# Kernel optimization log

Measured on AMD Instinct MI355X. Metric: run time of the kernel, lower is better.

## Reference

```python
import jax, jax.numpy as jnp
import numpy as np

N_NODES = 1395
NEG_SLOPE = 0.2


def gcn_conv(x, edge_index, W, b):
    # PyG GCNConv: add self-loops, symmetric deg^{-1/2} normalization,
    # out[i] = sum_j norm_ij * (x W)[j] + b
    N = x.shape[0]
    loop = jnp.arange(N, dtype=edge_index.dtype)
    src = jnp.concatenate([edge_index[0], loop])
    dst = jnp.concatenate([edge_index[1], loop])
    xw = x @ W  # [N, out]
    deg = jax.ops.segment_sum(jnp.ones_like(dst, dtype=x.dtype), dst, num_segments=N)
    dinv = jnp.where(deg > 0, deg ** -0.5, 0.0)
    norm = dinv[src] * dinv[dst]  # [E+N]
    out = jax.ops.segment_sum(xw[src] * norm[:, None], dst, num_segments=N)
    return out + b


def leaky_relu(x):
    return jnp.where(x >= 0, x, NEG_SLOPE * x)


def linear(v, W, b):
    # torch Linear on 1D vector: W @ v + b, W is [out, in]
    return W @ v + b


def conv2d(x, w, b):
    # x: [N,C,H,W], w: [O,I,kh,kw], valid padding, stride 1
    y = jax.lax.conv_general_dilated(
        x, w, window_strides=(1, 1), padding='VALID',
        dimension_numbers=('NCHW', 'OIHW', 'NCHW'))
    return y + b[None, :, None, None]


def _xavier(key, shape, fan_in, fan_out):
    a = float(np.sqrt(6.0 / (fan_in + fan_out)))
    return jax.random.uniform(key, shape, jnp.float32, -a, a)


def setup_inputs() -> dict:
    key = jax.random.key(0)
    ks = jax.random.split(key, 16)
    E = 44640
    x = jax.random.normal(ks[0], (N_NODES, 6), jnp.float32)
    edge_index = jax.random.randint(ks[1], (2, E), 0, N_NODES, jnp.int64)
    inp = {'x': x, 'edge_index': edge_index}
    inp['W1'] = _xavier(ks[2], (6, 3), 6, 3)
    inp['b1'] = jnp.zeros((3,), jnp.float32)
    inp['W2'] = _xavier(ks[3], (3, 3), 3, 3)
    inp['b2'] = jnp.zeros((3,), jnp.float32)
    inp['fc1_w'] = _xavier(ks[4], (2048, 4185), 4185, 2048)
    inp['fc1_b'] = jnp.zeros((2048,), jnp.float32)
    inp['fc2_w'] = _xavier(ks[5], (4096, 2048), 2048, 4096)
    inp['fc2_b'] = jnp.zeros((4096,), jnp.float32)
    inp['c1_w'] = _xavier(ks[6], (32, 1, 7, 7), 1 * 49, 32 * 49)
    inp['c1_b'] = jnp.zeros((32,), jnp.float32)
    inp['c2_w'] = _xavier(ks[7], (32, 32, 5, 5), 32 * 25, 32 * 25)
    inp['c2_b'] = jnp.zeros((32,), jnp.float32)
    inp['c3_w'] = _xavier(ks[8], (64, 32, 3, 3), 32 * 9, 64 * 9)
    inp['c3_b'] = jnp.zeros((64,), jnp.float32)
    inp['c4_w'] = _xavier(ks[9], (64, 64, 3, 3), 64 * 9, 64 * 9)
    inp['c4_b'] = jnp.zeros((64,), jnp.float32)
    inp['fc3_w'] = _xavier(ks[10], (2048, 160000), 160000, 2048)
    inp['fc3_b'] = jnp.zeros((2048,), jnp.float32)
    inp['fc4_w'] = _xavier(ks[11], (2048, 2048), 2048, 2048)
    inp['fc4_b'] = jnp.zeros((2048,), jnp.float32)
    inp['fc5_w'] = _xavier(ks[12], (48, 2048), 2048, 48)
    inp['fc5_b'] = jnp.zeros((48,), jnp.float32)
    return inp


def reference(x, edge_index, W1, b1, W2, b2, fc1_w, fc1_b, fc2_w, fc2_b,
              c1_w, c1_b, c2_w, c2_b, c3_w, c3_b, c4_w, c4_b,
              fc3_w, fc3_b, fc4_w, fc4_b, fc5_w, fc5_b):
    x = x.at[:, :3].set(0.0)
    h = leaky_relu(gcn_conv(x, edge_index, W1, b1))
    h = leaky_relu(gcn_conv(h, edge_index, W2, b2))
    v = h.reshape(-1)  # [4185]
    v = linear(v, fc1_w, fc1_b)
    v = linear(v, fc2_w, fc2_b)
    img = v.reshape(64, 64)[None, None]  # [1,1,64,64]
    img = conv2d(img, c1_w, c1_b)  # [1,32,58,58]
    img = conv2d(img, c2_w, c2_b)  # [1,32,54,54]
    img = conv2d(img, c3_w, c3_b)  # [1,64,52,52]
    img = conv2d(img, c4_w, c4_b)  # [1,64,50,50]
    v = linear(img.reshape(-1), fc3_w, fc3_b)
    v = linear(v, fc4_w, fc4_b)
    v = linear(v, fc5_w, fc5_b)
    return v
```

## Files before the change

kernel.cpp:

```cpp
#include <hip/hip_runtime.h>

#define NEG_SLOPE 0.2f
static const int N_NODES = 1395;
static const int N_EDGES = 44640;


__global__ void k_prep(const float* __restrict__ x, const float* __restrict__ W1,
                       float* __restrict__ xw1, float* __restrict__ deg,
                       float* __restrict__ acc1, float* __restrict__ acc2, int N) {
    int i = blockIdx.x * blockDim.x + threadIdx.x;
    if (i >= N) return;
    float x3 = x[i * 6 + 3], x4 = x[i * 6 + 4], x5 = x[i * 6 + 5];
#pragma unroll
    for (int j = 0; j < 3; ++j) {
        xw1[i * 3 + j] = x3 * W1[3 * 3 + j] + x4 * W1[4 * 3 + j] + x5 * W1[5 * 3 + j];
        acc1[i * 3 + j] = 0.f;
        acc2[i * 3 + j] = 0.f;
    }
    deg[i] = 0.f;
}

__global__ void k_deg(const int* __restrict__ ei, float* __restrict__ deg, int E) {
    int e = blockIdx.x * blockDim.x + threadIdx.x;
    if (e >= E) return;
    atomicAdd(&deg[ei[E + e]], 1.0f);
}

__global__ void k_dinv(float* __restrict__ deg, int N) {
    int i = blockIdx.x * blockDim.x + threadIdx.x;
    if (i >= N) return;
    deg[i] = 1.0f / sqrtf(deg[i] + 1.0f);
}

__global__ void k_scatter(const int* __restrict__ ei, const float* __restrict__ dinv,
                          const float* __restrict__ xw, float* __restrict__ acc, int E) {
    int e = blockIdx.x * blockDim.x + threadIdx.x;
    if (e >= E) return;
    int s = ei[e], d = ei[E + e];
    float w = dinv[s] * dinv[d];
    atomicAdd(&acc[d * 3 + 0], w * xw[s * 3 + 0]);
    atomicAdd(&acc[d * 3 + 1], w * xw[s * 3 + 1]);
    atomicAdd(&acc[d * 3 + 2], w * xw[s * 3 + 2]);
}

__global__ void k_node2(const float* __restrict__ acc1, const float* __restrict__ dinv,
                        const float* __restrict__ xw1, const float* __restrict__ b1,
                        const float* __restrict__ W2, float* __restrict__ xw2, int N) {
    int i = blockIdx.x * blockDim.x + threadIdx.x;
    if (i >= N) return;
    float di2 = dinv[i] * dinv[i];
    float h[3];
#pragma unroll
    for (int j = 0; j < 3; ++j) {
        float t = acc1[i * 3 + j] + di2 * xw1[i * 3 + j] + b1[j];
        h[j] = t >= 0.f ? t : NEG_SLOPE * t;
    }
#pragma unroll
    for (int j = 0; j < 3; ++j)
        xw2[i * 3 + j] = h[0] * W2[0 * 3 + j] + h[1] * W2[1 * 3 + j] + h[2] * W2[2 * 3 + j];
}

__global__ void k_node3(const float* __restrict__ acc2, const float* __restrict__ dinv,
                        const float* __restrict__ xw2, const float* __restrict__ b2,
                        float* __restrict__ v, int N) {
    int i = blockIdx.x * blockDim.x + threadIdx.x;
    if (i >= N) return;
    float di2 = dinv[i] * dinv[i];
#pragma unroll
    for (int j = 0; j < 3; ++j) {
        float t = acc2[i * 3 + j] + di2 * xw2[i * 3 + j] + b2[j];
        v[i * 3 + j] = t >= 0.f ? t : NEG_SLOPE * t;
    }
}


__device__ __forceinline__ float block_reduce_sum(float s) {
#pragma unroll
    for (int o = 32; o > 0; o >>= 1) s += __shfl_down(s, o, 64);
    __shared__ float parts[8];
    int lane = threadIdx.x & 63, wid = threadIdx.x >> 6;
    int nw = blockDim.x >> 6;
    if (lane == 0) parts[wid] = s;
    __syncthreads();
    if (threadIdx.x == 0) {
        for (int w = 1; w < nw; ++w) s += parts[w];
    }
    return s;
}

__global__ void k_gemv(const float* __restrict__ W, const float* __restrict__ x,
                       const float* __restrict__ b, float* __restrict__ y, int C) {
    int r = blockIdx.x;
    const float* row = W + (size_t)r * (size_t)C;
    float s = 0.f;
    for (int c = threadIdx.x; c < C; c += blockDim.x) s += row[c] * x[c];
    s = block_reduce_sum(s);
    if (threadIdx.x == 0) y[r] = s + b[r];
}

__global__ void k_gemv4(const float* __restrict__ W, const float* __restrict__ x,
                        const float* __restrict__ b, float* __restrict__ y, int C) {
    int r = blockIdx.x;
    const float4* row = (const float4*)(W + (size_t)r * (size_t)C);
    const float4* xv = (const float4*)x;
    int C4 = C >> 2;
    float s = 0.f;
    for (int c = threadIdx.x; c < C4; c += blockDim.x) {
        float4 a = row[c];
        float4 v = xv[c];
        s += a.x * v.x + a.y * v.y + a.z * v.z + a.w * v.w;
    }
    s = block_reduce_sum(s);
    if (threadIdx.x == 0) y[r] = s + b[r];
}

__global__ void k_conv(const float* __restrict__ in, const float* __restrict__ w,
                       const float* __restrict__ b, float* __restrict__ out,
                       int Cin, int H, int W, int K, int Hout, int Wout, int tilesPerCo) {
    int co = blockIdx.x / tilesPerCo;
    int tile = blockIdx.x % tilesPerCo;
    extern __shared__ float wl[];
    int wn = Cin * K * K;
    for (int t = threadIdx.x; t < wn; t += blockDim.x) wl[t] = w[co * wn + t];
    __syncthreads();
    int npix = Hout * Wout;
    float bias = b[co];
    for (int p = tile * blockDim.x + threadIdx.x; p < npix; p += tilesPerCo * blockDim.x) {
        int oh = p / Wout, ow = p - oh * Wout;
        float s = bias;
        const float* wp = wl;
        for (int ci = 0; ci < Cin; ++ci) {
            const float* ip = in + ((size_t)ci * H + oh) * W + ow;
            for (int kh = 0; kh < K; ++kh) {
#pragma unroll 4
                for (int kw = 0; kw < K; ++kw) s += ip[kh * W + kw] * wp[kh * K + kw];
            }
            wp += K * K;
        }
        out[((size_t)co * Hout + oh) * Wout + ow] = s;
    }
}


extern "C" void kernel_launch(void* const* d_in, const int* in_sizes, int n_in,
                              void* d_out, int out_size, void* d_ws, size_t ws_size,
                              hipStream_t stream) {
    const float* x      = (const float*)d_in[0];
    const int*   ei     = (const int*)d_in[1];
    const float* W1     = (const float*)d_in[2];
    const float* b1     = (const float*)d_in[3];
    const float* W2     = (const float*)d_in[4];
    const float* b2     = (const float*)d_in[5];
    const float* fc1_w  = (const float*)d_in[6];
    const float* fc1_b  = (const float*)d_in[7];
    const float* fc2_w  = (const float*)d_in[8];
    const float* fc2_b  = (const float*)d_in[9];
    const float* c1_w   = (const float*)d_in[10];
    const float* c1_b   = (const float*)d_in[11];
    const float* c2_w   = (const float*)d_in[12];
    const float* c2_b   = (const float*)d_in[13];
    const float* c3_w   = (const float*)d_in[14];
    const float* c3_b   = (const float*)d_in[15];
    const float* c4_w   = (const float*)d_in[16];
    const float* c4_b   = (const float*)d_in[17];
    const float* fc3_w  = (const float*)d_in[18];
    const float* fc3_b  = (const float*)d_in[19];
    const float* fc4_w  = (const float*)d_in[20];
    const float* fc4_b  = (const float*)d_in[21];
    const float* fc5_w  = (const float*)d_in[22];
    const float* fc5_b  = (const float*)d_in[23];
    float* out = (float*)d_out;

    float* ws = (float*)d_ws;
    size_t off = 0;
    auto alloc = [&](size_t n) { float* p = ws + off; off += (n + 3) & ~(size_t)3; return p; };
    const int N = N_NODES, E = N_EDGES;
    float* deg  = alloc(N);
    float* xw1  = alloc(N * 3);
    float* acc1 = alloc(N * 3);
    float* xw2  = alloc(N * 3);
    float* acc2 = alloc(N * 3);
    float* v    = alloc(4185);
    float* y1   = alloc(2048);
    float* y2   = alloc(4096);
    float* i1   = alloc(32 * 58 * 58);
    float* i2   = alloc(32 * 54 * 54);
    float* i3   = alloc(64 * 52 * 52);
    float* i4   = alloc(64 * 50 * 50);
    float* y3   = alloc(2048);
    float* y4   = alloc(2048);
    (void)ws_size; (void)in_sizes; (void)n_in; (void)out_size;

    int nb = (N + 255) / 256;
    int eb = (E + 255) / 256;

    k_prep<<<nb, 256, 0, stream>>>(x, W1, xw1, deg, acc1, acc2, N);
    k_deg<<<eb, 256, 0, stream>>>(ei, deg, E);
    k_dinv<<<nb, 256, 0, stream>>>(deg, N);
    k_scatter<<<eb, 256, 0, stream>>>(ei, deg, xw1, acc1, E);
    k_node2<<<nb, 256, 0, stream>>>(acc1, deg, xw1, b1, W2, xw2, N);
    k_scatter<<<eb, 256, 0, stream>>>(ei, deg, xw2, acc2, E);
    k_node3<<<nb, 256, 0, stream>>>(acc2, deg, xw2, b2, v, N);

    k_gemv<<<2048, 256, 0, stream>>>(fc1_w, v, fc1_b, y1, 4185);
    k_gemv4<<<4096, 256, 0, stream>>>(fc2_w, y1, fc2_b, y2, 2048);

    k_conv<<<32 * 8,  256, 1 * 7 * 7 * 4,   stream>>>(y2, c1_w, c1_b, i1, 1, 64, 64, 7, 58, 58, 8);
    k_conv<<<32 * 12, 256, 32 * 5 * 5 * 4,  stream>>>(i1, c2_w, c2_b, i2, 32, 58, 58, 5, 54, 54, 12);
    k_conv<<<64 * 11, 256, 32 * 3 * 3 * 4,  stream>>>(i2, c3_w, c3_b, i3, 32, 54, 54, 3, 52, 52, 11);
    k_conv<<<64 * 10, 256, 64 * 3 * 3 * 4,  stream>>>(i3, c4_w, c4_b, i4, 64, 52, 52, 3, 50, 50, 10);

    k_gemv4<<<2048, 256, 0, stream>>>(fc3_w, i4, fc3_b, y3, 160000);
    k_gemv4<<<2048, 256, 0, stream>>>(fc4_w, y3, fc4_b, y4, 2048);
    k_gemv4<<<48, 256, 0, stream>>>(fc5_w, y4, fc5_b, out, 2048);
}
```

Baseline: 1.985 ms.

## Split-K GEMVs with 4-way accumulators and templated unrolled convolutions

Large GEMVs (fc2, fc3, fc4) now split each row's reduction across several blocks that write partial sums, and a small finish kernel adds the partials and the bias. Each thread keeps four independent accumulators to raise memory-level parallelism. The fc1 GEMV gets the same multi-accumulator unroll. The convolution kernel is templated on kernel size so both inner loops fully unroll, and the conv tile counts are changed. The cost is extra kernel launches and a partial-sum buffer round trip.

Measured after the change: 1.882 ms. 5.2% less time.

```diff
diff --git a/kernel.cpp b/kernel.cpp
--- a/kernel.cpp
+++ b/kernel.cpp
@@ -92,9 +92,17 @@
                        const float* __restrict__ b, float* __restrict__ y, int C) {
     int r = blockIdx.x;
     const float* row = W + (size_t)r * (size_t)C;
-    float s = 0.f;
-    for (int c = threadIdx.x; c < C; c += blockDim.x) s += row[c] * x[c];
-    s = block_reduce_sum(s);
+    int step = blockDim.x;
+    float a0 = 0.f, a1 = 0.f, a2 = 0.f, a3 = 0.f;
+    int c = threadIdx.x;
+    for (; c + 3 * step < C; c += 4 * step) {
+        a0 += row[c] * x[c];
+        a1 += row[c + step] * x[c + step];
+        a2 += row[c + 2 * step] * x[c + 2 * step];
+        a3 += row[c + 3 * step] * x[c + 3 * step];
+    }
+    for (; c < C; c += step) a0 += row[c] * x[c];
+    float s = block_reduce_sum(a0 + a1 + a2 + a3);
     if (threadIdx.x == 0) y[r] = s + b[r];
 }
 
@@ -114,9 +122,47 @@
     if (threadIdx.x == 0) y[r] = s + b[r];
 }
 
+__global__ void k_gemv_part(const float* __restrict__ W, const float* __restrict__ x,
+                            float* __restrict__ partial, int C4, int S) {
+    int r = blockIdx.x / S, s = blockIdx.x % S;
+    int c0 = (int)(((long long)C4 * s) / S);
+    int c1 = (int)(((long long)C4 * (s + 1)) / S);
+    const float4* row = (const float4*)W + (size_t)r * (size_t)C4;
+    const float4* xv = (const float4*)x;
+    int step = blockDim.x;
+    float a0 = 0.f, a1 = 0.f, a2 = 0.f, a3 = 0.f;
+    int c = c0 + threadIdx.x;
+    for (; c + 3 * step < c1; c += 4 * step) {
+        float4 w0 = row[c];            float4 v0 = xv[c];
+        float4 w1 = row[c + step];     float4 v1 = xv[c + step];
+        float4 w2 = row[c + 2 * step]; float4 v2 = xv[c + 2 * step];
+        float4 w3 = row[c + 3 * step]; float4 v3 = xv[c + 3 * step];
+        a0 += w0.x * v0.x + w0.y * v0.y + w0.z * v0.z + w0.w * v0.w;
+        a1 += w1.x * v1.x + w1.y * v1.y + w1.z * v1.z + w1.w * v1.w;
+        a2 += w2.x * v2.x + w2.y * v2.y + w2.z * v2.z + w2.w * v2.w;
+        a3 += w3.x * v3.x + w3.y * v3.y + w3.z * v3.z + w3.w * v3.w;
+    }
+    for (; c < c1; c += step) {
+        float4 w0 = row[c]; float4 v0 = xv[c];
+        a0 += w0.x * v0.x + w0.y * v0.y + w0.z * v0.z + w0.w * v0.w;
+    }
+    float ssum = block_reduce_sum(a0 + a1 + a2 + a3);
+    if (threadIdx.x == 0) partial[r * S + s] = ssum;
+}
+
+__global__ void k_gemv_fin(const float* __restrict__ partial, const float* __restrict__ b,
+                           float* __restrict__ y, int R, int S) {
+    int r = blockIdx.x * blockDim.x + threadIdx.x;
+    if (r >= R) return;
+    float ssum = b[r];
+    for (int s = 0; s < S; ++s) ssum += partial[r * S + s];
+    y[r] = ssum;
+}
+
+template <int K>
 __global__ void k_conv(const float* __restrict__ in, const float* __restrict__ w,
                        const float* __restrict__ b, float* __restrict__ out,
-                       int Cin, int H, int W, int K, int Hout, int Wout, int tilesPerCo) {
+                       int Cin, int H, int W, int Hout, int Wout, int tilesPerCo) {
     int co = blockIdx.x / tilesPerCo;
     int tile = blockIdx.x % tilesPerCo;
     extern __shared__ float wl[];
@@ -131,8 +177,9 @@
         const float* wp = wl;
         for (int ci = 0; ci < Cin; ++ci) {
             const float* ip = in + ((size_t)ci * H + oh) * W + ow;
+#pragma unroll
             for (int kh = 0; kh < K; ++kh) {
-#pragma unroll 4
+#pragma unroll
                 for (int kw = 0; kw < K; ++kw) s += ip[kh * W + kw] * wp[kh * K + kw];
             }
             wp += K * K;
@@ -189,6 +236,7 @@
     float* i4   = alloc(64 * 50 * 50);
     float* y3   = alloc(2048);
     float* y4   = alloc(2048);
+    float* pbuf = alloc(2048 * 8);
     (void)ws_size; (void)in_sizes; (void)n_in; (void)out_size;
 
     int nb = (N + 255) / 256;
@@ -203,14 +251,17 @@
     k_node3<<<nb, 256, 0, stream>>>(acc2, deg, xw2, b2, v, N);
 
     k_gemv<<<2048, 256, 0, stream>>>(fc1_w, v, fc1_b, y1, 4185);
-    k_gemv4<<<4096, 256, 0, stream>>>(fc2_w, y1, fc2_b, y2, 2048);
-
-    k_conv<<<32 * 8,  256, 1 * 7 * 7 * 4,   stream>>>(y2, c1_w, c1_b, i1, 1, 64, 64, 7, 58, 58, 8);
-    k_conv<<<32 * 12, 256, 32 * 5 * 5 * 4,  stream>>>(i1, c2_w, c2_b, i2, 32, 58, 58, 5, 54, 54, 12);
-    k_conv<<<64 * 11, 256, 32 * 3 * 3 * 4,  stream>>>(i2, c3_w, c3_b, i3, 32, 54, 54, 3, 52, 52, 11);
-    k_conv<<<64 * 10, 256, 64 * 3 * 3 * 4,  stream>>>(i3, c4_w, c4_b, i4, 64, 52, 52, 3, 50, 50, 10);
-
-    k_gemv4<<<2048, 256, 0, stream>>>(fc3_w, i4, fc3_b, y3, 160000);
-    k_gemv4<<<2048, 256, 0, stream>>>(fc4_w, y3, fc4_b, y4, 2048);
+    k_gemv_part<<<4096 * 2, 256, 0, stream>>>(fc2_w, y1, pbuf, 2048 / 4, 2);
+    k_gemv_fin<<<(4096 + 255) / 256, 256, 0, stream>>>(pbuf, fc2_b, y2, 4096, 2);
+
+    k_conv<7><<<32 * 16, 256, 1 * 7 * 7 * 4,  stream>>>(y2, c1_w, c1_b, i1, 1, 64, 64, 58, 58, 16);
+    k_conv<5><<<32 * 16, 256, 32 * 5 * 5 * 4, stream>>>(i1, c2_w, c2_b, i2, 32, 58, 58, 54, 54, 16);
+    k_conv<3><<<64 * 8,  256, 32 * 3 * 3 * 4, stream>>>(i2, c3_w, c3_b, i3, 32, 54, 54, 52, 52, 8);
+    k_conv<3><<<64 * 8,  256, 64 * 3 * 3 * 4, stream>>>(i3, c4_w, c4_b, i4, 64, 52, 52, 50, 50, 8);
+
+    k_gemv_part<<<2048 * 8, 256, 0, stream>>>(fc3_w, i4, pbuf, 160000 / 4, 8);
+    k_gemv_fin<<<(2048 + 255) / 256, 256, 0, stream>>>(pbuf, fc3_b, y3, 2048, 8);
+    k_gemv_part<<<2048 * 2, 256, 0, stream>>>(fc4_w, y3, pbuf, 2048 / 4, 2);
+    k_gemv_fin<<<(2048 + 255) / 256, 256, 0, stream>>>(pbuf, fc4_b, y4, 2048, 2);
     k_gemv4<<<48, 256, 0, stream>>>(fc5_w, y4, fc5_b, out, 2048);
 }
```
